# Performance work log

Measured on AMD Instinct MI355X. Metric: run time of the kernel, lower is better.

The kernel has to match this reference:

```python
import jax, jax.numpy as jnp
import numpy as np

B, C, F = 262144, 64, 256
N_ITERS = 8


def setup_inputs() -> dict:
    key = jax.random.key(0)
    ks = jax.random.split(key, 8)
    s = lambda fan_in: 1.0 / np.sqrt(fan_in)
    return {
        "y": jax.random.normal(ks[0], (B, C), jnp.float32),
        "log_det_jacobians": jnp.zeros((B,), jnp.float32),
        "v": jax.random.normal(ks[1], (B, 1, C), jnp.float32),
        "W1": jax.random.normal(ks[2], (F, C), jnp.float32) * s(C),
        "b1": jnp.zeros((F,), jnp.float32),
        "W2": jax.random.normal(ks[3], (F, F), jnp.float32) * s(F),
        "b2": jnp.zeros((F,), jnp.float32),
        "W3": jax.random.normal(ks[4], (C, F), jnp.float32) * s(F),
        "b3": jnp.zeros((C,), jnp.float32),
    }


def reference(y, log_det_jacobians, v, W1, b1, W2, b2, W3, b3):
    def mlp(t):
        h = jax.nn.elu(t)
        h = jax.nn.elu(h @ W1.T + b1)
        h = jax.nn.elu(h @ W2.T + b2)
        return h @ W3.T + b3  # [B, C]

    g_y, vjp_fn = jax.vjp(mlp, y)
    v0 = v[:, 0, :]  # n_samples = 1
    w = v0
    log_det = jnp.zeros((y.shape[0],), y.dtype)
    for k in range(1, N_ITERS + 1):
        w = vjp_fn(w)[0]              # w <- w @ J, J = dg/dy
        inner = jnp.einsum('bd,bd->b', w, v0)
        # torch code: add when (k+1) % 2 == 0 (k odd), subtract when k even
        log_det = log_det + (inner / k if (k + 1) % 2 == 0 else -inner / k)

    z = y + g_y
    return z, log_det_jacobians + log_det
```

## Files before the change

### kernel.cpp

```cpp
#include <hip/hip_runtime.h>

#define BN 262144

typedef short bf16x8 __attribute__((ext_vector_type(8)));
typedef float f32x4 __attribute__((ext_vector_type(4)));
typedef unsigned int u32x2 __attribute__((ext_vector_type(2)));

#define MFMA16(a,b,c) __builtin_amdgcn_mfma_f32_16x16x32_bf16((a),(b),(c),0,0,0)

__device__ __forceinline__ unsigned short f2bf(float f) {
  union { float f; unsigned int u; } x; x.f = f;
  unsigned int u = x.u + 0x7fffu + ((x.u >> 16) & 1u);
  return (unsigned short)(u >> 16);
}
__device__ __forceinline__ float bf2f(unsigned int h) {
  union { unsigned int u; float f; } x; x.u = h << 16;
  return x.f;
}
__device__ __forceinline__ unsigned pk2(float lo, float hi) {
  union { float f; unsigned int u; } a, b; a.f = lo; b.f = hi;
  return (a.u >> 16) | (b.u & 0xffff0000u);
}
__device__ __forceinline__ unsigned swz(int row) {
  return (((unsigned)(row & 7)) << 4) ^ (((unsigned)(row & 8)) << 2);
}

#define O_R1 0
#define O_R2 16384
#define O_R3 81920
#define O_R4 98304
#define O_R5 114688
#define O_R6 180224
#define N_WS 196608

__global__ void invres_prep(const float* __restrict__ W1, const float* __restrict__ W2,
                            const float* __restrict__ W3, unsigned short* __restrict__ wsb) {
  int idx = blockIdx.x * 256 + threadIdx.x;
  if (idx >= N_WS) return;
  int j = idx & 7;
  int lane = (idx >> 3) & 63;
  int nn = lane & 15, kn = (lane >> 4) * 8 + j;
  float val;
  if (idx < O_R2) {
    int g = idx >> 9; int s = g & 1; int ct = g >> 1;
    val = W1[(ct * 16 + nn) * 64 + (s * 32 + kn)];
  } else if (idx < O_R3) {
    int g = (idx - O_R2) >> 9; int s = g & 7; int ct = g >> 3;
    val = W2[(ct * 16 + nn) * 256 + (s * 32 + kn)];
  } else if (idx < O_R4) {
    int g = (idx - O_R3) >> 9; int s = g & 7; int ct = g >> 3;
    val = W3[(ct * 16 + nn) * 256 + (s * 32 + kn)];
  } else if (idx < O_R5) {
    int g = (idx - O_R4) >> 9; int s = g & 1; int ct = g >> 1;
    val = W3[(s * 32 + kn) * 256 + (ct * 16 + nn)];
  } else if (idx < O_R6) {
    int g = (idx - O_R5) >> 9; int s = g & 7; int ct = g >> 3;
    val = W2[(s * 32 + kn) * 256 + (ct * 16 + nn)];
  } else {
    int g = (idx - O_R6) >> 9; int s = g & 7; int ct = g >> 3;
    val = W1[(s * 32 + kn) * 64 + (ct * 16 + nn)];
  }
  wsb[idx] = f2bf(val);
}

#define L_PB  16384
#define L_WB  32768
#define L_D1  36864
#define L_D2  53248
#define L_LDP 69632
#define L_SIZE 70144

__global__ void __launch_bounds__(512, 4)
invres_main(const float* __restrict__ y, const float* __restrict__ ldj,
            const float* __restrict__ v, const float* __restrict__ b1,
            const float* __restrict__ b2, const float* __restrict__ b3,
            const unsigned short* __restrict__ wsb, float* __restrict__ out) {
  extern __shared__ char smem[];
  char* PA = smem;
  char* PB = smem + L_PB;
  char* WB = smem + L_WB;
  char* D1 = smem + L_D1;
  char* D2 = smem + L_D2;
  float* ldp = (float*)(smem + L_LDP);

  const int tid = threadIdx.x;
  const int lane = tid & 63;
  const int wid = tid >> 6;
  const int l15 = lane & 15, g16 = lane >> 4;
  const int ct0 = wid * 2;
  const int mh = wid >> 2;
  const int ctn = wid & 3;
  const int r0 = blockIdx.x * 32;

  const bf16x8* R1 = (const bf16x8*)(wsb + O_R1);
  const bf16x8* R2 = (const bf16x8*)(wsb + O_R2);
  const bf16x8* R3 = (const bf16x8*)(wsb + O_R3);
  const bf16x8* R4 = (const bf16x8*)(wsb + O_R4);
  const bf16x8* R5 = (const bf16x8*)(wsb + O_R5);
  const bf16x8* R6 = (const bf16x8*)(wsb + O_R6);

  auto mOff = [&](int mc) -> int { return ((wid * 4 + mc) * 64 + lane) * 8; };

  auto ldsA = [&](const char* buf, int mm, int s) -> bf16x8 {
    int row = mm * 16 + l15;
    unsigned byte = ((unsigned)(s * 64 + g16 * 16)) ^ swz(row);
    return *(const bf16x8*)(buf + row * 512 + byte);
  };
  auto stage64 = [&](char* buf, int mm, int cc, const float* hv) {
    int row = mm * 16 + l15;
    unsigned byte = ((unsigned)(((ct0 + cc) * 16 + g16 * 4) * 2)) ^ swz(row);
    u32x2 w; w[0] = pk2(hv[0], hv[1]); w[1] = pk2(hv[2], hv[3]);
    *(u32x2*)(buf + row * 512 + byte) = w;
  };
  auto gA = [&](const float* p, int mm, int s, bool elu) -> bf16x8 {
    const float* q = p + (size_t)(r0 + mm * 16 + l15) * 64 + s * 32 + g16 * 8;
    f32x4 a = __builtin_nontemporal_load((const f32x4*)q);
    f32x4 b = __builtin_nontemporal_load((const f32x4*)(q + 4));
    float xv[8] = {a[0], a[1], a[2], a[3], b[0], b[1], b[2], b[3]};
    bf16x8 f;
#pragma unroll
    for (int i = 0; i < 8; i++) {
      float x = xv[i];
      if (elu) x = x > 0.f ? x : (__expf(x) - 1.f);
      f[i] = (short)f2bf(x);
    }
    return f;
  };

  f32x4 bv1[2], bv2[2], bv3;
#pragma unroll
  for (int cc = 0; cc < 2; cc++) {
    bv1[cc] = *(const f32x4*)(b1 + (ct0 + cc) * 16 + g16 * 4);
    bv2[cc] = *(const f32x4*)(b2 + (ct0 + cc) * 16 + g16 * 4);
  }
  bv3 = *(const f32x4*)(b3 + ctn * 16 + g16 * 4);

  unsigned d0p[2], v0p[2];
  float ldacc[4] = {0.f, 0.f, 0.f, 0.f};

  {
    f32x4 acc[2][2] = {};
#pragma unroll
    for (int s = 0; s < 2; s++) {
      bf16x8 a0 = gA(y, 0, s, true);
      bf16x8 a1 = gA(y, 1, s, true);
#pragma unroll
      for (int cc = 0; cc < 2; cc++) {
        bf16x8 B = R1[((ct0 + cc) * 2 + s) * 64 + lane];
        acc[0][cc] = MFMA16(B, a0, acc[0][cc]);
        acc[1][cc] = MFMA16(B, a1, acc[1][cc]);
      }
    }
#pragma unroll
    for (int mm = 0; mm < 2; mm++)
#pragma unroll
      for (int cc = 0; cc < 2; cc++) {
        float hv[4], dv[4];
#pragma unroll
        for (int r = 0; r < 4; r++) {
          float a = acc[mm][cc][r] + bv1[cc][r];
          float e = __expf(a);
          hv[r] = a > 0.f ? a : (e - 1.f);
          dv[r] = a > 0.f ? 1.f : e;
        }
        stage64(PA, mm, cc, hv);
        u32x2 w; w[0] = pk2(dv[0], dv[1]); w[1] = pk2(dv[2], dv[3]);
        *(u32x2*)(D1 + mOff(mm * 2 + cc)) = w;
      }
  }
  __syncthreads();

  {
    f32x4 acc[2][2] = {};
    bf16x8 a0 = ldsA(PA, 0, 0);
    bf16x8 a1 = ldsA(PA, 1, 0);
#pragma unroll 1
    for (int s = 0; s < 8; s++) {
      bf16x8 c0 = a0, c1 = a1;
      int sn = s < 7 ? s + 1 : 7;
      a0 = ldsA(PA, 0, sn);
      a1 = ldsA(PA, 1, sn);
      bf16x8 B0 = R2[(ct0 * 8 + s) * 64 + lane];
      bf16x8 B1 = R2[((ct0 + 1) * 8 + s) * 64 + lane];
      acc[0][0] = MFMA16(B0, c0, acc[0][0]);
      acc[0][1] = MFMA16(B1, c0, acc[0][1]);
      acc[1][0] = MFMA16(B0, c1, acc[1][0]);
      acc[1][1] = MFMA16(B1, c1, acc[1][1]);
    }
#pragma unroll
    for (int mm = 0; mm < 2; mm++)
#pragma unroll
      for (int cc = 0; cc < 2; cc++) {
        float hv[4], dv[4];
#pragma unroll
        for (int r = 0; r < 4; r++) {
          float a = acc[mm][cc][r] + bv2[cc][r];
          float e = __expf(a);
          hv[r] = a > 0.f ? a : (e - 1.f);
          dv[r] = a > 0.f ? 1.f : e;
        }
        stage64(PB, mm, cc, hv);
        u32x2 w; w[0] = pk2(dv[0], dv[1]); w[1] = pk2(dv[2], dv[3]);
        *(u32x2*)(D2 + mOff(mm * 2 + cc)) = w;
      }
  }
  __syncthreads();

  {
    f32x4 acc0 = {}, acc1 = {};
    bf16x8 p0 = ldsA(PB, mh, 0);
    bf16x8 p1 = ldsA(PB, mh, 1);
#pragma unroll 1
    for (int s = 0; s < 8; s += 2) {
      bf16x8 c0 = p0, c1 = p1;
      int sn = s + 2 < 8 ? s + 2 : 0;
      p0 = ldsA(PB, mh, sn);
      p1 = ldsA(PB, mh, sn + 1);
      acc0 = MFMA16(R3[(ctn * 8 + s) * 64 + lane], c0, acc0);
      acc1 = MFMA16(R3[(ctn * 8 + s + 1) * 64 + lane], c1, acc1);
    }
    int row = r0 + mh * 16 + l15;
    int col = ctn * 16 + g16 * 4;
    size_t off = (size_t)row * 64 + col;
    f32x4 yv = __builtin_nontemporal_load((const f32x4*)(y + off));
    f32x4 vv = __builtin_nontemporal_load((const f32x4*)(v + off));
    f32x4 zv;
    float d0v[4];
#pragma unroll
    for (int r = 0; r < 4; r++) {
      zv[r] = yv[r] + acc0[r] + acc1[r] + bv3[r];
      d0v[r] = yv[r] > 0.f ? 1.f : __expf(yv[r]);
    }
    __builtin_nontemporal_store(zv, (f32x4*)(out + off));
    d0p[0] = pk2(d0v[0], d0v[1]); d0p[1] = pk2(d0v[2], d0v[3]);
    v0p[0] = pk2(vv[0], vv[1]);   v0p[1] = pk2(vv[2], vv[3]);
  }

  {
    f32x4 acc[2][2] = {};
#pragma unroll
    for (int s = 0; s < 2; s++) {
      bf16x8 a0 = gA(v, 0, s, false);
      bf16x8 a1 = gA(v, 1, s, false);
#pragma unroll
      for (int cc = 0; cc < 2; cc++) {
        bf16x8 B = R4[((ct0 + cc) * 2 + s) * 64 + lane];
        acc[0][cc] = MFMA16(B, a0, acc[0][cc]);
        acc[1][cc] = MFMA16(B, a1, acc[1][cc]);
      }
    }
#pragma unroll
    for (int mm = 0; mm < 2; mm++)
#pragma unroll
      for (int cc = 0; cc < 2; cc++) {
        u32x2 dd = *(const u32x2*)(D2 + mOff(mm * 2 + cc));
        float uv[4];
#pragma unroll
        for (int r = 0; r < 4; r++)
          uv[r] = acc[mm][cc][r] * bf2f((dd[r >> 1] >> ((r & 1) * 16)) & 0xffffu);
        stage64(PA, mm, cc, uv);
      }
  }
  __syncthreads();

  for (int k = 1; k <= 8; ++k) {
    {
      f32x4 acc[2][2] = {};
      bf16x8 a0 = ldsA(PA, 0, 0);
      bf16x8 a1 = ldsA(PA, 1, 0);
#pragma unroll 1
      for (int s = 0; s < 8; s++) {
        bf16x8 c0 = a0, c1 = a1;
        int sn = s < 7 ? s + 1 : 7;
        a0 = ldsA(PA, 0, sn);
        a1 = ldsA(PA, 1, sn);
        bf16x8 B0 = R5[(ct0 * 8 + s) * 64 + lane];
        bf16x8 B1 = R5[((ct0 + 1) * 8 + s) * 64 + lane];
        acc[0][0] = MFMA16(B0, c0, acc[0][0]);
        acc[0][1] = MFMA16(B1, c0, acc[0][1]);
        acc[1][0] = MFMA16(B0, c1, acc[1][0]);
        acc[1][1] = MFMA16(B1, c1, acc[1][1]);
      }
#pragma unroll
      for (int mm = 0; mm < 2; mm++)
#pragma unroll
        for (int cc = 0; cc < 2; cc++) {
          u32x2 dd = *(const u32x2*)(D1 + mOff(mm * 2 + cc));
          float uv[4];
#pragma unroll
          for (int r = 0; r < 4; r++)
            uv[r] = acc[mm][cc][r] * bf2f((dd[r >> 1] >> ((r & 1) * 16)) & 0xffffu);
          stage64(PB, mm, cc, uv);
        }
    }
    __syncthreads();

    {
      float coef = (k & 1) ? (1.f / (float)k) : (-1.f / (float)k);
      f32x4 acc0 = {}, acc1 = {};
      bf16x8 p0 = ldsA(PB, mh, 0);
      bf16x8 p1 = ldsA(PB, mh, 1);
#pragma unroll 1
      for (int s = 0; s < 8; s += 2) {
        bf16x8 c0 = p0, c1 = p1;
        int sn = s + 2 < 8 ? s + 2 : 0;
        p0 = ldsA(PB, mh, sn);
        p1 = ldsA(PB, mh, sn + 1);
        acc0 = MFMA16(R6[(ctn * 8 + s) * 64 + lane], c0, acc0);
        acc1 = MFMA16(R6[(ctn * 8 + s + 1) * 64 + lane], c1, acc1);
      }
      float wv[4];
#pragma unroll
      for (int r = 0; r < 4; r++) {
        wv[r] = (acc0[r] + acc1[r]) * bf2f((d0p[r >> 1] >> ((r & 1) * 16)) & 0xffffu);
        ldacc[r] += coef * wv[r] * bf2f((v0p[r >> 1] >> ((r & 1) * 16)) & 0xffffu);
      }
      if (k < 8) {
        int row = mh * 16 + l15;
        unsigned byte = ((unsigned)((ctn * 16 + g16 * 4) * 2)) ^ swz(row);
        u32x2 w; w[0] = pk2(wv[0], wv[1]); w[1] = pk2(wv[2], wv[3]);
        *(u32x2*)(WB + row * 128 + byte) = w;
      }
    }
    if (k < 8) {
      __syncthreads();
      f32x4 acc[2][2] = {};
#pragma unroll
      for (int s = 0; s < 2; s++) {
        bf16x8 a0, a1;
#pragma unroll
        for (int mm = 0; mm < 2; mm++) {
          int row = mm * 16 + l15;
          unsigned byte = ((unsigned)(s * 64 + g16 * 16)) ^ swz(row);
          bf16x8 a = *(const bf16x8*)(WB + row * 128 + byte);
          if (mm == 0) a0 = a; else a1 = a;
        }
#pragma unroll
        for (int cc = 0; cc < 2; cc++) {
          bf16x8 B = R4[((ct0 + cc) * 2 + s) * 64 + lane];
          acc[0][cc] = MFMA16(B, a0, acc[0][cc]);
          acc[1][cc] = MFMA16(B, a1, acc[1][cc]);
        }
      }
#pragma unroll
      for (int mm = 0; mm < 2; mm++)
#pragma unroll
        for (int cc = 0; cc < 2; cc++) {
          u32x2 dd = *(const u32x2*)(D2 + mOff(mm * 2 + cc));
          float uv[4];
#pragma unroll
          for (int r = 0; r < 4; r++)
            uv[r] = acc[mm][cc][r] * bf2f((dd[r >> 1] >> ((r & 1) * 16)) & 0xffffu);
          stage64(PA, mm, cc, uv);
        }
      __syncthreads();
    }
  }

  {
    float s = ldacc[0] + ldacc[1] + ldacc[2] + ldacc[3];
    s += __shfl_xor(s, 16);
    s += __shfl_xor(s, 32);
    if (g16 == 0) ldp[(mh * 16 + l15) * 4 + ctn] = s;
  }
  __syncthreads();
  if (tid < 32) {
    float s = ldp[tid * 4] + ldp[tid * 4 + 1] + ldp[tid * 4 + 2] + ldp[tid * 4 + 3];
    int gb = r0 + tid;
    __builtin_nontemporal_store(ldj[gb] + s, out + (size_t)BN * 64 + gb);
  }
}

extern "C" void kernel_launch(void* const* d_in, const int* in_sizes, int n_in,
                              void* d_out, int out_size, void* d_ws, size_t ws_size,
                              hipStream_t stream) {
  const float* y   = (const float*)d_in[0];
  const float* ldj = (const float*)d_in[1];
  const float* v   = (const float*)d_in[2];
  const float* W1  = (const float*)d_in[3];
  const float* b1  = (const float*)d_in[4];
  const float* W2  = (const float*)d_in[5];
  const float* b2  = (const float*)d_in[6];
  const float* W3  = (const float*)d_in[7];
  const float* b3  = (const float*)d_in[8];
  unsigned short* wsb = (unsigned short*)d_ws;
  float* out = (float*)d_out;

  (void)hipFuncSetAttribute(reinterpret_cast<const void*>(&invres_main),
                            hipFuncAttributeMaxDynamicSharedMemorySize, L_SIZE);

  invres_prep<<<N_WS / 256, 256, 0, stream>>>(W1, W2, W3, wsb);
  invres_main<<<BN / 32, 512, L_SIZE, stream>>>(y, ldj, v, b1, b2, b3, wsb, out);
}
```

Baseline: 806.4 us.

## Merge ping-pong LDS activation buffers into one to raise occupancy to six blocks

Replaces the two separate PA/PB activation staging buffers with a single shared buffer, adding __syncthreads barriers between reading and overwriting it, which cuts LDS per block from about 70KB to about 54KB. Launch bounds are raised from 4 to 6 blocks per CU to use the freed LDS and registers. Bias loads move into the stages that use them and the software-prefetch of the next LDS fragment is dropped, both to lower register pressure. In exchange it adds extra barriers per stage and loses the LDS prefetch overlap, and tighter register limits could cause spills.

```diff
diff --git a/kernel.cpp b/kernel.cpp
--- a/kernel.cpp
+++ b/kernel.cpp
@@ -63,21 +63,19 @@
   wsb[idx] = f2bf(val);
 }
 
-#define L_PB  16384
-#define L_WB  32768
-#define L_D1  36864
-#define L_D2  53248
-#define L_LDP 69632
-#define L_SIZE 70144
-
-__global__ void __launch_bounds__(512, 4)
+#define L_WB  16384
+#define L_D1  20480
+#define L_D2  36864
+#define L_LDP 53248
+#define L_SIZE 53760
+
+__global__ void __launch_bounds__(512, 6)
 invres_main(const float* __restrict__ y, const float* __restrict__ ldj,
             const float* __restrict__ v, const float* __restrict__ b1,
             const float* __restrict__ b2, const float* __restrict__ b3,
             const unsigned short* __restrict__ wsb, float* __restrict__ out) {
   extern __shared__ char smem[];
-  char* PA = smem;
-  char* PB = smem + L_PB;
+  char* P  = smem;
   char* WB = smem + L_WB;
   char* D1 = smem + L_D1;
   char* D2 = smem + L_D2;
@@ -127,18 +125,13 @@
     return f;
   };
 
-  f32x4 bv1[2], bv2[2], bv3;
-#pragma unroll
-  for (int cc = 0; cc < 2; cc++) {
-    bv1[cc] = *(const f32x4*)(b1 + (ct0 + cc) * 16 + g16 * 4);
-    bv2[cc] = *(const f32x4*)(b2 + (ct0 + cc) * 16 + g16 * 4);
-  }
-  bv3 = *(const f32x4*)(b3 + ctn * 16 + g16 * 4);
-
   unsigned d0p[2], v0p[2];
   float ldacc[4] = {0.f, 0.f, 0.f, 0.f};
 
   {
+    f32x4 bv1[2];
+#pragma unroll
+    for (int cc = 0; cc < 2; cc++) bv1[cc] = *(const f32x4*)(b1 + (ct0 + cc) * 16 + g16 * 4);
     f32x4 acc[2][2] = {};
 #pragma unroll
     for (int s = 0; s < 2; s++) {
@@ -163,7 +156,7 @@
           hv[r] = a > 0.f ? a : (e - 1.f);
           dv[r] = a > 0.f ? 1.f : e;
         }
-        stage64(PA, mm, cc, hv);
+        stage64(P, mm, cc, hv);
         u32x2 w; w[0] = pk2(dv[0], dv[1]); w[1] = pk2(dv[2], dv[3]);
         *(u32x2*)(D1 + mOff(mm * 2 + cc)) = w;
       }
@@ -172,21 +165,21 @@
 
   {
     f32x4 acc[2][2] = {};
-    bf16x8 a0 = ldsA(PA, 0, 0);
-    bf16x8 a1 = ldsA(PA, 1, 0);
 #pragma unroll 1
     for (int s = 0; s < 8; s++) {
-      bf16x8 c0 = a0, c1 = a1;
-      int sn = s < 7 ? s + 1 : 7;
-      a0 = ldsA(PA, 0, sn);
-      a1 = ldsA(PA, 1, sn);
+      bf16x8 a0 = ldsA(P, 0, s);
+      bf16x8 a1 = ldsA(P, 1, s);
       bf16x8 B0 = R2[(ct0 * 8 + s) * 64 + lane];
       bf16x8 B1 = R2[((ct0 + 1) * 8 + s) * 64 + lane];
-      acc[0][0] = MFMA16(B0, c0, acc[0][0]);
-      acc[0][1] = MFMA16(B1, c0, acc[0][1]);
-      acc[1][0] = MFMA16(B0, c1, acc[1][0]);
-      acc[1][1] = MFMA16(B1, c1, acc[1][1]);
-    }
+      acc[0][0] = MFMA16(B0, a0, acc[0][0]);
+      acc[0][1] = MFMA16(B1, a0, acc[0][1]);
+      acc[1][0] = MFMA16(B0, a1, acc[1][0]);
+      acc[1][1] = MFMA16(B1, a1, acc[1][1]);
+    }
+    __syncthreads();
+    f32x4 bv2[2];
+#pragma unroll
+    for (int cc = 0; cc < 2; cc++) bv2[cc] = *(const f32x4*)(b2 + (ct0 + cc) * 16 + g16 * 4);
 #pragma unroll
     for (int mm = 0; mm < 2; mm++)
 #pragma unroll
@@ -199,7 +192,7 @@
           hv[r] = a > 0.f ? a : (e - 1.f);
           dv[r] = a > 0.f ? 1.f : e;
         }
-        stage64(PB, mm, cc, hv);
+        stage64(P, mm, cc, hv);
         u32x2 w; w[0] = pk2(dv[0], dv[1]); w[1] = pk2(dv[2], dv[3]);
         *(u32x2*)(D2 + mOff(mm * 2 + cc)) = w;
       }
@@ -208,17 +201,12 @@
 
   {
     f32x4 acc0 = {}, acc1 = {};
-    bf16x8 p0 = ldsA(PB, mh, 0);
-    bf16x8 p1 = ldsA(PB, mh, 1);
 #pragma unroll 1
     for (int s = 0; s < 8; s += 2) {
-      bf16x8 c0 = p0, c1 = p1;
-      int sn = s + 2 < 8 ? s + 2 : 0;
-      p0 = ldsA(PB, mh, sn);
-      p1 = ldsA(PB, mh, sn + 1);
-      acc0 = MFMA16(R3[(ctn * 8 + s) * 64 + lane], c0, acc0);
-      acc1 = MFMA16(R3[(ctn * 8 + s + 1) * 64 + lane], c1, acc1);
-    }
+      acc0 = MFMA16(R3[(ctn * 8 + s) * 64 + lane], ldsA(P, mh, s), acc0);
+      acc1 = MFMA16(R3[(ctn * 8 + s + 1) * 64 + lane], ldsA(P, mh, s + 1), acc1);
+    }
+    f32x4 bv3 = *(const f32x4*)(b3 + ctn * 16 + g16 * 4);
     int row = r0 + mh * 16 + l15;
     int col = ctn * 16 + g16 * 4;
     size_t off = (size_t)row * 64 + col;
@@ -235,6 +223,7 @@
     d0p[0] = pk2(d0v[0], d0v[1]); d0p[1] = pk2(d0v[2], d0v[3]);
     v0p[0] = pk2(vv[0], vv[1]);   v0p[1] = pk2(vv[2], vv[3]);
   }
+  __syncthreads();
 
   {
     f32x4 acc[2][2] = {};
@@ -258,7 +247,7 @@
 #pragma unroll
         for (int r = 0; r < 4; r++)
           uv[r] = acc[mm][cc][r] * bf2f((dd[r >> 1] >> ((r & 1) * 16)) & 0xffffu);
-        stage64(PA, mm, cc, uv);
+        stage64(P, mm, cc, uv);
       }
   }
   __syncthreads();
@@ -266,21 +255,18 @@
   for (int k = 1; k <= 8; ++k) {
     {
       f32x4 acc[2][2] = {};
-      bf16x8 a0 = ldsA(PA, 0, 0);
-      bf16x8 a1 = ldsA(PA, 1, 0);
 #pragma unroll 1
       for (int s = 0; s < 8; s++) {
-        bf16x8 c0 = a0, c1 = a1;
-        int sn = s < 7 ? s + 1 : 7;
-        a0 = ldsA(PA, 0, sn);
-        a1 = ldsA(PA, 1, sn);
+        bf16x8 a0 = ldsA(P, 0, s);
+        bf16x8 a1 = ldsA(P, 1, s);
         bf16x8 B0 = R5[(ct0 * 8 + s) * 64 + lane];
         bf16x8 B1 = R5[((ct0 + 1) * 8 + s) * 64 + lane];
-        acc[0][0] = MFMA16(B0, c0, acc[0][0]);
-        acc[0][1] = MFMA16(B1, c0, acc[0][1]);
-        acc[1][0] = MFMA16(B0, c1, acc[1][0]);
-        acc[1][1] = MFMA16(B1, c1, acc[1][1]);
-      }
+        acc[0][0] = MFMA16(B0, a0, acc[0][0]);
+        acc[0][1] = MFMA16(B1, a0, acc[0][1]);
+        acc[1][0] = MFMA16(B0, a1, acc[1][0]);
+        acc[1][1] = MFMA16(B1, a1, acc[1][1]);
+      }
+      __syncthreads();
 #pragma unroll
       for (int mm = 0; mm < 2; mm++)
 #pragma unroll
@@ -290,7 +276,7 @@
 #pragma unroll
           for (int r = 0; r < 4; r++)
             uv[r] = acc[mm][cc][r] * bf2f((dd[r >> 1] >> ((r & 1) * 16)) & 0xffffu);
-          stage64(PB, mm, cc, uv);
+          stage64(P, mm, cc, uv);
         }
     }
     __syncthreads();
@@ -298,16 +284,10 @@
     {
       float coef = (k & 1) ? (1.f / (float)k) : (-1.f / (float)k);
       f32x4 acc0 = {}, acc1 = {};
-      bf16x8 p0 = ldsA(PB, mh, 0);
-      bf16x8 p1 = ldsA(PB, mh, 1);
 #pragma unroll 1
       for (int s = 0; s < 8; s += 2) {
-        bf16x8 c0 = p0, c1 = p1;
-        int sn = s + 2 < 8 ? s + 2 : 0;
-        p0 = ldsA(PB, mh, sn);
-        p1 = ldsA(PB, mh, sn + 1);
-        acc0 = MFMA16(R6[(ctn * 8 + s) * 64 + lane], c0, acc0);
-        acc1 = MFMA16(R6[(ctn * 8 + s + 1) * 64 + lane], c1, acc1);
+        acc0 = MFMA16(R6[(ctn * 8 + s) * 64 + lane], ldsA(P, mh, s), acc0);
+        acc1 = MFMA16(R6[(ctn * 8 + s + 1) * 64 + lane], ldsA(P, mh, s + 1), acc1);
       }
       float wv[4];
 #pragma unroll
@@ -351,7 +331,7 @@
 #pragma unroll
           for (int r = 0; r < 4; r++)
             uv[r] = acc[mm][cc][r] * bf2f((dd[r >> 1] >> ((r & 1) * 16)) & 0xffffu);
-          stage64(PA, mm, cc, uv);
+          stage64(P, mm, cc, uv);
         }
       __syncthreads();
     }
```

Result: faster. 781.6 us (-3.1%).
